# Optimization experiments

Hardware: AMD Instinct MI355X
Metric: run time of the kernel (lower is better)

## Reference

```python
import jax, jax.numpy as jnp
import numpy as np

N_HEAD = 50000
N_TAIL = 50000
E = 1600000
IN_F = 256
OUT_F = 32
NHEAD = 4
EDGE_F = 64
N_ETYPES = 5
NEG_SLOPE = 0.2


def setup_inputs() -> dict:
    key = jax.random.key(0)
    ks = jax.random.split(key, 10)
    return {
        "head_feature": jax.random.normal(ks[0], (N_HEAD, IN_F), jnp.float32),
        "tail_feature": jax.random.normal(ks[1], (N_TAIL, IN_F), jnp.float32),
        "W": jax.random.normal(ks[2], (IN_F, OUT_F * NHEAD), jnp.float32) * 0.05,
        "W_e": jax.random.normal(ks[3], (EDGE_F, EDGE_F * NHEAD), jnp.float32) * 0.05,
        "edge_emb": jax.random.normal(ks[4], (N_ETYPES, EDGE_F), jnp.float32) * 0.1,
        "a_l": jax.random.normal(ks[5], (1, NHEAD, OUT_F), jnp.float32) * 0.1,
        "a_r": jax.random.normal(ks[6], (1, NHEAD, OUT_F), jnp.float32) * 0.1,
        "a_e": jax.random.normal(ks[7], (1, NHEAD, EDGE_F), jnp.float32) * 0.1,
        "edge_list": jax.random.randint(ks[8], (2, E), 0, N_HEAD, jnp.int64),
        "tmp_edge": jax.random.randint(ks[9], (E,), 0, N_ETYPES, jnp.int64),
    }


def reference(head_feature, tail_feature, W, W_e, edge_emb, a_l, a_r, a_e, edge_list, tmp_edge):
    n_head_nodes = head_feature.shape[0]
    nhead, out_dim = a_l.shape[1], a_l.shape[2]
    edge_feats = a_e.shape[2]

    # dense projections (dropout in eval mode = identity)
    h_head = (head_feature @ W).reshape(-1, nhead, out_dim)   # [Nh, H, D]
    h_tail = (tail_feature @ W).reshape(-1, nhead, out_dim)   # [Nt, H, D]
    e = (edge_emb @ W_e).reshape(-1, nhead, edge_feats)       # [T,  H, De]

    head_ind = edge_list[0]
    tail_ind = edge_list[1]

    # per-edge attention logits [E, H]
    h_e = (a_e * e).sum(-1)[tmp_edge]
    h_l = (a_l * h_head).sum(-1)[head_ind]
    h_r = (a_r * h_tail).sum(-1)[tail_ind]
    att = jax.nn.leaky_relu(h_l + h_r + h_e, negative_slope=NEG_SLOPE)

    # sparse softmax over dim=1 (per head-node row), per head
    m = jax.ops.segment_max(att, head_ind, num_segments=n_head_nodes)
    m = jnp.where(jnp.isfinite(m), m, jnp.zeros_like(m))  # empty rows
    ex = jnp.exp(att - m[head_ind])
    denom = jax.ops.segment_sum(ex, head_ind, num_segments=n_head_nodes)
    alpha = ex / denom[head_ind]                              # [E, H]

    # sparse-mm aggregation: out[i] = sum_e alpha_e * h_tail[tail_e]
    msg = alpha[..., None] * h_tail[tail_ind]                 # [E, H, D]
    out = jax.ops.segment_sum(msg, head_ind, num_segments=n_head_nodes)
    out = out.reshape(n_head_nodes, nhead * out_dim)
    out = jax.nn.elu(out)
    return out, alpha
```

## Files before the change

### kernel.cpp

```cpp
#include <hip/hip_runtime.h>
#include <hip/hip_bf16.h>
#include <string.h>

#define NNODE 50000
#define NEDGE 1600000
#define INF   256
#define NH    4
#define EF    64
#define NET   5

#define NBUCK 782
#define BCAP  2560
#define EPB   2048
#define PBLK  782
#define BKS   784
#define RDB   1563

typedef unsigned short u16t;
typedef __attribute__((ext_vector_type(8))) short short8;
typedef __attribute__((ext_vector_type(4))) float f32x4;

__device__ __forceinline__ float b2f(u16t u) {
    union { unsigned int i; float f; } v; v.i = ((unsigned int)u) << 16; return v.f;
}
__device__ __forceinline__ u16t f2b(float f) {
    __hip_bfloat16 h = __float2bfloat16(f);
    u16t u; memcpy(&u, &h, 2); return u;
}

__global__ void k_detect(const int* __restrict__ el, const int* __restrict__ ety,
                         int* __restrict__ flag) {
    int tid = threadIdx.x;
    int w = tid >> 6, lane = tid & 63;
    const int* p = (w == 0) ? el : ety;
    int x = p[2 * lane + 1];
    unsigned long long b = __ballot(x != 0);
    if (lane == 0) flag[w] = (b == 0ULL) ? 1 : 0;
}

__global__ void k_prep(const float* __restrict__ W, const float* __restrict__ We,
                       const float* __restrict__ emb, const float* __restrict__ al,
                       const float* __restrict__ ar, const float* __restrict__ ae,
                       float* __restrict__ wl, float* __restrict__ wr,
                       float* __restrict__ he) {
    __shared__ float wes[EF * NH];
    int tid = threadIdx.x;
    {
        int k = tid;
        for (int h = 0; h < NH; h++) {
            float accl = 0.f, accr = 0.f;
            for (int d = 0; d < 32; d++) {
                float w = W[k * 128 + h * 32 + d];
                accl += w * al[h * 32 + d];
                accr += w * ar[h * 32 + d];
            }
            wl[k * NH + h] = accl;
            wr[k * NH + h] = accr;
        }
    }
    if (tid < EF) {
        int k = tid;
        for (int h = 0; h < NH; h++) {
            float s = 0.f;
            for (int d = 0; d < EF; d++)
                s += We[k * (NH * EF) + h * EF + d] * ae[h * EF + d];
            wes[k * NH + h] = s;
        }
    }
    __syncthreads();
    if (tid < NET * NH) {
        int t = tid / NH, h = tid % NH;
        float s = 0.f;
        for (int k = 0; k < EF; k++)
            s += emb[t * EF + k] * wes[k * NH + h];
        he[tid] = s;
    }
}

__global__ void k_prepw(const float* __restrict__ W, u16t* __restrict__ Wfrag) {
    int idx = blockIdx.x * 256 + threadIdx.x;
    int j    = idx & 7;
    int lane = (idx >> 3) & 63;
    int ks   = (idx >> 9) & 7;
    int tile = idx >> 12;
    int n = tile * 16 + (lane & 15);
    int k = ks * 32 + (lane >> 4) * 8 + j;
    Wfrag[idx] = f2b(W[k * 128 + n]);
}

__global__ void k_fuseA(const float* __restrict__ head, const float* __restrict__ tail,
                        const float* __restrict__ wl, const float* __restrict__ wr,
                        const int* __restrict__ el, const int* __restrict__ ety,
                        const int* __restrict__ flag,
                        int* __restrict__ hist2d, int* __restrict__ loff2d,
                        unsigned int* __restrict__ bucketbuf,
                        float* __restrict__ hl, float* __restrict__ hr) {
    __shared__ unsigned int srec[EPB];
    __shared__ int hist[BKS];
    __shared__ int loff[BKS];
    __shared__ int psum[256];
    int b = blockIdx.x;
    int tid = threadIdx.x;
    if (b < PBLK) {
        int base = b * EPB;
        int wf = flag[0], wt = flag[1];
        for (int i = tid; i < BKS; i += 256) hist[i] = 0;
        __syncthreads();
        unsigned int rec[8];
        unsigned int br[8];
#pragma unroll
        for (int i = 0; i < 8; i++) {
            int e = base + i * 256 + tid;
            br[i] = 0xffffffffu;
            rec[i] = 0;
            if (e < NEDGE) {
                int hi = wf ? el[2 * (long long)e]           : el[e];
                int ti = wf ? el[2 * ((long long)NEDGE + e)] : el[NEDGE + e];
                int ty = wt ? ety[2 * (long long)e]          : ety[e];
                int bk = hi >> 6;
                int r = atomicAdd(&hist[bk], 1);
                rec[i] = (unsigned)ti | ((unsigned)(hi & 63) << 16) | ((unsigned)ty << 22);
                br[i]  = (unsigned)bk | ((unsigned)r << 16);
            }
        }
        __syncthreads();
        int s4[4]; int tsum = 0;
        if (tid < 196) {
#pragma unroll
            for (int j = 0; j < 4; j++) { s4[j] = hist[4 * tid + j]; tsum += s4[j]; }
        }
        psum[tid] = (tid < 196) ? tsum : 0;
        __syncthreads();
        for (int off = 1; off < 256; off <<= 1) {
            int v = (tid >= off) ? psum[tid - off] : 0;
            __syncthreads();
            psum[tid] += v;
            __syncthreads();
        }
        if (tid < 196) {
            int run = tid ? psum[tid - 1] : 0;
#pragma unroll
            for (int j = 0; j < 4; j++) {
                int bk = 4 * tid + j;
                loff[bk] = run;
                hist2d[b * BKS + bk] = s4[j];
                loff2d[b * BKS + bk] = run;
                run += s4[j];
            }
        }
        __syncthreads();
#pragma unroll
        for (int i = 0; i < 8; i++) {
            if (br[i] != 0xffffffffu) {
                int bk = br[i] & 0xffff;
                int r  = br[i] >> 16;
                srec[loff[bk] + r] = rec[i];
            }
        }
        __syncthreads();
        int tot = psum[255];
        for (int i = tid; i < tot; i += 256)
            bucketbuf[(size_t)b * EPB + i] = srec[i];
    } else {
        int bb = b - PBLK;
        int ishead = (bb < RDB);
        const float* X  = ishead ? head : tail;
        const float* wv = ishead ? wl : wr;
        float* o        = ishead ? hl : hr;
        int rowbase = (ishead ? bb : bb - RDB) * 32;
        int wave = tid >> 6;
        int g = (tid >> 4) & 3;
        int l = tid & 15;
        const float4* wv4 = (const float4*)wv;
        float4 acc[2];
#pragma unroll
        for (int rr = 0; rr < 2; rr++) {
            acc[rr].x = 0.f; acc[rr].y = 0.f; acc[rr].z = 0.f; acc[rr].w = 0.f;
            int row = rowbase + rr * 16 + wave * 4 + g;
            if (row < NNODE) {
                const float* xp = X + (size_t)row * INF + l * 4;
#pragma unroll
                for (int c = 0; c < 4; c++) {
                    float4 xv = *(const float4*)(xp + c * 64);
                    float xs[4] = {xv.x, xv.y, xv.z, xv.w};
#pragma unroll
                    for (int j = 0; j < 4; j++) {
                        float4 wvv = wv4[c * 64 + l * 4 + j];
                        acc[rr].x += xs[j] * wvv.x;
                        acc[rr].y += xs[j] * wvv.y;
                        acc[rr].z += xs[j] * wvv.z;
                        acc[rr].w += xs[j] * wvv.w;
                    }
                }
            }
        }
#pragma unroll
        for (int rr = 0; rr < 2; rr++) {
#pragma unroll
            for (int off = 8; off > 0; off >>= 1) {
                acc[rr].x += __shfl_xor(acc[rr].x, off);
                acc[rr].y += __shfl_xor(acc[rr].y, off);
                acc[rr].z += __shfl_xor(acc[rr].z, off);
                acc[rr].w += __shfl_xor(acc[rr].w, off);
            }
            int row = rowbase + rr * 16 + wave * 4 + g;
            if (l == 0 && row < NNODE) ((float4*)o)[row] = acc[rr];
        }
    }
}

__global__ void k_bsum(const int* __restrict__ hist2d, int* __restrict__ cursor) {
    __shared__ int red[256];
    int bk = blockIdx.x;
    int tid = threadIdx.x;
    int s = 0;
    for (int sb = tid; sb < PBLK; sb += 256) s += hist2d[sb * BKS + bk];
    red[tid] = s;
    __syncthreads();
    for (int off = 128; off > 0; off >>= 1) {
        if (tid < off) red[tid] += red[tid + off];
        __syncthreads();
    }
    if (tid == 0) cursor[bk] = red[0];
}

__global__ void k_bscan(const int* __restrict__ cursor, int* __restrict__ bstart,
                        int* __restrict__ row_start) {
    __shared__ int psum[256];
    int tid = threadIdx.x;
    int s4[4]; int tsum = 0;
    if (tid < 196) {
#pragma unroll
        for (int j = 0; j < 4; j++) {
            int bk = 4 * tid + j;
            s4[j] = (bk < NBUCK) ? cursor[bk] : 0;
            tsum += s4[j];
        }
    }
    psum[tid] = (tid < 196) ? tsum : 0;
    __syncthreads();
    for (int off = 1; off < 256; off <<= 1) {
        int v = (tid >= off) ? psum[tid - off] : 0;
        __syncthreads();
        psum[tid] += v;
        __syncthreads();
    }
    if (tid < 196) {
        int run = tid ? psum[tid - 1] : 0;
#pragma unroll
        for (int j = 0; j < 4; j++) {
            int bk = 4 * tid + j;
            if (bk < NBUCK) bstart[bk] = run;
            run += s4[j];
        }
    }
    if (tid == 255) {
        bstart[NBUCK] = psum[255];
        row_start[NNODE] = psum[255];
    }
}

__global__ void k_fuseB(const float* __restrict__ X, const u16t* __restrict__ Wfrag,
                        u16t* __restrict__ H, const unsigned int* __restrict__ bucketbuf,
                        const int* __restrict__ hist2d, const int* __restrict__ loff2d,
                        const int* __restrict__ bstart,
                        unsigned int* __restrict__ cpack, int* __restrict__ row_start) {
    __shared__ __attribute__((aligned(16))) u16t alds[16 * 264];
    __shared__ unsigned int lrec[BCAP];
    __shared__ unsigned int lord[BCAP];
    __shared__ int psum[256];
    __shared__ int cnt[64];
    __shared__ int sc[64];
    int b = blockIdx.x;
    int tid = threadIdx.x;
    if (b < 3125) {
        int rowbase = b * 16;
        for (int i = tid; i < 1024; i += 256) {
            int row = i >> 6;
            int kc = (i & 63) * 4;
            float4 v = *(const float4*)(X + (size_t)(rowbase + row) * INF + kc);
            u16t* d = alds + row * 264 + kc;
            d[0] = f2b(v.x); d[1] = f2b(v.y); d[2] = f2b(v.z); d[3] = f2b(v.w);
        }
        __syncthreads();
        int wave = tid >> 6, lane = tid & 63;
        int m = lane & 15, quad = lane >> 4;
        int t0 = wave * 2, t1 = t0 + 1;
        f32x4 acc0 = {0.f, 0.f, 0.f, 0.f};
        f32x4 acc1 = {0.f, 0.f, 0.f, 0.f};
#pragma unroll
        for (int ks = 0; ks < 8; ks++) {
            short8 a  = *(const short8*)(alds + m * 264 + ks * 32 + quad * 8);
            short8 b0 = *(const short8*)(Wfrag + (((t0 * 8 + ks) * 64 + lane) << 3));
            short8 b1 = *(const short8*)(Wfrag + (((t1 * 8 + ks) * 64 + lane) << 3));
            acc0 = __builtin_amdgcn_mfma_f32_16x16x32_bf16(a, b0, acc0, 0, 0, 0);
            acc1 = __builtin_amdgcn_mfma_f32_16x16x32_bf16(a, b1, acc1, 0, 0, 0);
        }
        u16t* Hp = H + (size_t)rowbase * 128;
#pragma unroll
        for (int r = 0; r < 4; r++) {
            int row = quad * 4 + r;
            Hp[(size_t)row * 128 + t0 * 16 + m] = f2b(acc0[r]);
            Hp[(size_t)row * 128 + t1 * 16 + m] = f2b(acc1[r]);
        }
    } else {
        int q = b - 3125;
        int bs = bstart[q];
        int c4[4], o4[4]; int tsum = 0;
        if (tid < 196) {
#pragma unroll
            for (int j = 0; j < 4; j++) {
                int sb = 4 * tid + j;
                c4[j] = 0; o4[j] = 0;
                if (sb < PBLK) {
                    c4[j] = hist2d[sb * BKS + q];
                    o4[j] = loff2d[sb * BKS + q];
                }
                tsum += c4[j];
            }
        }
        psum[tid] = (tid < 196) ? tsum : 0;
        __syncthreads();
        for (int off = 1; off < 256; off <<= 1) {
            int v = (tid >= off) ? psum[tid - off] : 0;
            __syncthreads();
            psum[tid] += v;
            __syncthreads();
        }
        if (tid < 196) {
            int run = tid ? psum[tid - 1] : 0;
#pragma unroll
            for (int j = 0; j < 4; j++) {
                int sb = 4 * tid + j;
                for (int k = 0; k < c4[j]; k++) {
                    int d = run + k;
                    if (d < BCAP)
                        lrec[d] = bucketbuf[(size_t)sb * EPB + o4[j] + k];
                }
                run += c4[j];
            }
        }
        if (tid < 64) cnt[tid] = 0;
        __syncthreads();
        int nrec = psum[255];
        if (nrec > BCAP) nrec = BCAP;
        unsigned int myr[10];
        int k2 = 0;
        for (int i = tid; i < nrec; i += 256) {
            int n = (lrec[i] >> 16) & 63;
            myr[k2++] = atomicAdd(&cnt[n], 1);
        }
        __syncthreads();
        if (tid < 64) sc[tid] = cnt[tid];
        __syncthreads();
        for (int off = 1; off < 64; off <<= 1) {
            int v = (tid >= off && tid < 64) ? sc[tid - off] : 0;
            __syncthreads();
            if (tid < 64) sc[tid] += v;
            __syncthreads();
        }
        k2 = 0;
        for (int i = tid; i < nrec; i += 256) {
            unsigned int rc = lrec[i];
            int n  = (rc >> 16) & 63;
            int ti = rc & 0xffff;
            int ty = rc >> 22;
            int pos = (sc[n] - cnt[n]) + (int)myr[k2++];
            lord[pos] = ((unsigned)ty << 18) | (unsigned)ti;
        }
        __syncthreads();
        for (int i = tid; i < nrec; i += 256)
            cpack[bs + i] = lord[i];
        if (tid < 64) {
            int node = q * 64 + tid;
            if (node < NNODE) row_start[node] = bs + (sc[tid] - cnt[tid]);
        }
    }
}

__global__ void k_agg(const int* __restrict__ rs, const unsigned int* __restrict__ cpack,
                      const float* __restrict__ hl, const float* __restrict__ hr,
                      const float* __restrict__ heg, const u16t* __restrict__ ht,
                      float* __restrict__ den, float2* __restrict__ out) {
    __shared__ float hes[NET * NH];
    int tid = threadIdx.x;
    if (tid < NET * NH) hes[tid] = heg[tid];
    __syncthreads();
    int wave = tid >> 6, lane = tid & 63;
    int node = blockIdx.x * 4 + wave;
    int start = rs[node], end = rs[node + 1];
    unsigned h = (unsigned)(lane >> 4);
    unsigned lane2 = (unsigned)(lane << 1);
    float hlv = hl[(unsigned)node * 4u + h];
    const float* hesh = hes + h;
    float a0 = 0.f, a1 = 0.f, s = 0.f;
    int j = start;
    for (; j + 4 <= end; j += 4) {
        unsigned c0 = cpack[j], c1 = cpack[j + 1], c2 = cpack[j + 2], c3 = cpack[j + 3];
        unsigned t0 = c0 & 0xffffu, t1 = c1 & 0xffffu;
        unsigned t2 = c2 & 0xffffu, t3 = c3 & 0xffffu;
        float r0 = hr[(t0 << 2) + h], r1 = hr[(t1 << 2) + h];
        float r2 = hr[(t2 << 2) + h], r3 = hr[(t3 << 2) + h];
        unsigned v0 = *(const unsigned*)(ht + ((t0 << 7) + lane2));
        unsigned v1 = *(const unsigned*)(ht + ((t1 << 7) + lane2));
        unsigned v2 = *(const unsigned*)(ht + ((t2 << 7) + lane2));
        unsigned v3 = *(const unsigned*)(ht + ((t3 << 7) + lane2));
        float x0 = hlv + r0 + hesh[c0 >> 16];
        float x1 = hlv + r1 + hesh[c1 >> 16];
        float x2 = hlv + r2 + hesh[c2 >> 16];
        float x3 = hlv + r3 + hesh[c3 >> 16];
        x0 = fmaxf(x0, 0.2f * x0);
        x1 = fmaxf(x1, 0.2f * x1);
        x2 = fmaxf(x2, 0.2f * x2);
        x3 = fmaxf(x3, 0.2f * x3);
        float e0 = __expf(x0), e1 = __expf(x1), e2 = __expf(x2), e3 = __expf(x3);
        union { unsigned u; float f; } w0, w1;
        w0.u = v0 << 16;          w1.u = v0 & 0xffff0000u;
        a0 += e0 * w0.f;          a1 += e0 * w1.f;
        w0.u = v1 << 16;          w1.u = v1 & 0xffff0000u;
        a0 += e1 * w0.f;          a1 += e1 * w1.f;
        w0.u = v2 << 16;          w1.u = v2 & 0xffff0000u;
        a0 += e2 * w0.f;          a1 += e2 * w1.f;
        w0.u = v3 << 16;          w1.u = v3 & 0xffff0000u;
        a0 += e3 * w0.f;          a1 += e3 * w1.f;
        s  += e0 + e1 + e2 + e3;
    }
    for (; j < end; j++) {
        unsigned c = cpack[j];
        unsigned ti = c & 0xffffu;
        float att = hlv + hr[(ti << 2) + h] + hesh[c >> 16];
        att = fmaxf(att, 0.2f * att);
        float exv = __expf(att);
        unsigned hv = *(const unsigned*)(ht + ((ti << 7) + lane2));
        union { unsigned u; float f; } w0, w1;
        w0.u = hv << 16;  w1.u = hv & 0xffff0000u;
        a0 += exv * w0.f;
        a1 += exv * w1.f;
        s  += exv;
    }
    if ((lane & 15) == 0) den[(unsigned)node * 4u + h] = s;
    float o0 = 0.f, o1 = 0.f;
    if (s > 0.f) { o0 = a0 / s; o1 = a1 / s; }
    o0 = o0 > 0.f ? o0 : expm1f(o0);
    o1 = o1 > 0.f ? o1 : expm1f(o1);
    float2 ov = {o0, o1};
    out[(size_t)node * 64 + lane] = ov;
}

__global__ void k_alpha(const int* __restrict__ el, const int* __restrict__ ety,
                        const int* __restrict__ flag,
                        const float* __restrict__ hl, const float* __restrict__ hr,
                        const float* __restrict__ heg, const float* __restrict__ den,
                        float* __restrict__ alpha) {
    __shared__ float hes[NET * NH];
    int tid = threadIdx.x;
    if (tid < NET * NH) hes[tid] = heg[tid];
    __syncthreads();
    int wf = flag[0], wt = flag[1];
    int e = blockIdx.x * 256 + tid;
    int hi = wf ? el[2 * (long long)e]           : el[e];
    int ti = wf ? el[2 * ((long long)NEDGE + e)] : el[NEDGE + e];
    int ty = wt ? ety[2 * (long long)e]          : ety[e];
    float4 l = ((const float4*)hl)[hi];
    float4 r = ((const float4*)hr)[ti];
    float4 d = ((const float4*)den)[hi];
    float v0 = l.x + r.x + hes[ty * 4 + 0];
    float v1 = l.y + r.y + hes[ty * 4 + 1];
    float v2 = l.z + r.z + hes[ty * 4 + 2];
    float v3 = l.w + r.w + hes[ty * 4 + 3];
    v0 = v0 > 0.f ? v0 : 0.2f * v0;
    v1 = v1 > 0.f ? v1 : 0.2f * v1;
    v2 = v2 > 0.f ? v2 : 0.2f * v2;
    v3 = v3 > 0.f ? v3 : 0.2f * v3;
    float4 o;
    o.x = d.x > 0.f ? __expf(v0) / d.x : 0.f;
    o.y = d.y > 0.f ? __expf(v1) / d.y : 0.f;
    o.z = d.z > 0.f ? __expf(v2) / d.z : 0.f;
    o.w = d.w > 0.f ? __expf(v3) / d.w : 0.f;
    ((float4*)alpha)[e] = o;
}

extern "C" void kernel_launch(void* const* d_in, const int* in_sizes, int n_in,
                              void* d_out, int out_size, void* d_ws, size_t ws_size,
                              hipStream_t stream) {
    const float* head = (const float*)d_in[0];
    const float* tail = (const float*)d_in[1];
    const float* W    = (const float*)d_in[2];
    const float* We   = (const float*)d_in[3];
    const float* emb  = (const float*)d_in[4];
    const float* al   = (const float*)d_in[5];
    const float* ar   = (const float*)d_in[6];
    const float* ae   = (const float*)d_in[7];
    const int*   el   = (const int*)d_in[8];
    const int*   ety  = (const int*)d_in[9];

    float* ws = (float*)d_ws;
    float* hl       = ws;
    float* hr       = ws + 200000;
    float* wl       = ws + 400000;
    float* wr       = ws + 401024;
    float* heg      = ws + 402048;
    int*   flag     = (int*)(ws + 402080);
    int*   bstart   = (int*)(ws + 402096);
    int*   cursor   = (int*)(ws + 402880);
    float* den      = ws + 403664;
    int*   row_start= (int*)(ws + 603664);
    u16t*  Wfrag    = (u16t*)(ws + 653668);

    float* outp   = (float*)d_out;
    float* alphap = (float*)d_out + 6400000;
    u16t*         htail = (u16t*)alphap;
    unsigned int* cpack = (unsigned int*)(alphap + 3200000);
    unsigned int* bucketbuf = (unsigned int*)outp;
    int* hist2d = (int*)outp + 1601536;
    int* loff2d = hist2d + 613088;

    k_detect<<<1, 128, 0, stream>>>(el, ety, flag);
    k_prep<<<1, 256, 0, stream>>>(W, We, emb, al, ar, ae, wl, wr, heg);
    k_prepw<<<128, 256, 0, stream>>>(W, Wfrag);
    k_fuseA<<<PBLK + 2 * RDB, 256, 0, stream>>>(head, tail, wl, wr, el, ety, flag,
                                                hist2d, loff2d, bucketbuf, hl, hr);
    k_bsum<<<NBUCK, 256, 0, stream>>>(hist2d, cursor);
    k_bscan<<<1, 256, 0, stream>>>(cursor, bstart, row_start);
    k_fuseB<<<3125 + NBUCK, 256, 0, stream>>>(tail, Wfrag, htail, bucketbuf,
                                              hist2d, loff2d, bstart, cpack, row_start);
    k_agg<<<NNODE / 4, 256, 0, stream>>>(row_start, cpack, hl, hr, heg, htail,
                                         den, (float2*)outp);
    k_alpha<<<NEDGE / 256, 256, 0, stream>>>(el, ety, flag, hl, hr, heg, den, alphap);
}
```

Before: 338.4 us.

## Merge prep kernels and compute tail logits from the MFMA projection output

The three small setup kernels (flag detection, logit-weight prep, W fragment packing) are merged into one launch with block-specialised roles. The tail-node attention term hr is no longer computed by a separate pass over tail_feature in k_fuseA. Instead k_fuseB takes the dot product of a_r with the MFMA accumulators it already holds, cutting one full read of tail features and two launches. The catch is that hr is now derived from a bf16-input projection rather than fp32, which slightly changes numerics.

```diff
diff --git a/kernel.cpp b/kernel.cpp
--- a/kernel.cpp
+++ b/kernel.cpp
@@ -28,73 +28,74 @@
     u16t u; memcpy(&u, &h, 2); return u;
 }
 
-__global__ void k_detect(const int* __restrict__ el, const int* __restrict__ ety,
-                         int* __restrict__ flag) {
-    int tid = threadIdx.x;
-    int w = tid >> 6, lane = tid & 63;
-    const int* p = (w == 0) ? el : ety;
-    int x = p[2 * lane + 1];
-    unsigned long long b = __ballot(x != 0);
-    if (lane == 0) flag[w] = (b == 0ULL) ? 1 : 0;
-}
-
-__global__ void k_prep(const float* __restrict__ W, const float* __restrict__ We,
-                       const float* __restrict__ emb, const float* __restrict__ al,
-                       const float* __restrict__ ar, const float* __restrict__ ae,
-                       float* __restrict__ wl, float* __restrict__ wr,
-                       float* __restrict__ he) {
-    __shared__ float wes[EF * NH];
-    int tid = threadIdx.x;
-    {
-        int k = tid;
-        for (int h = 0; h < NH; h++) {
-            float accl = 0.f, accr = 0.f;
-            for (int d = 0; d < 32; d++) {
-                float w = W[k * 128 + h * 32 + d];
-                accl += w * al[h * 32 + d];
-                accr += w * ar[h * 32 + d];
-            }
-            wl[k * NH + h] = accl;
-            wr[k * NH + h] = accr;
-        }
-    }
-    if (tid < EF) {
-        int k = tid;
-        for (int h = 0; h < NH; h++) {
+__global__ void k_pre(const float* __restrict__ W, const float* __restrict__ We,
+                      const float* __restrict__ emb, const float* __restrict__ al,
+                      const float* __restrict__ ar, const float* __restrict__ ae,
+                      const int* __restrict__ el, const int* __restrict__ ety,
+                      float* __restrict__ wl, float* __restrict__ wr,
+                      float* __restrict__ he, int* __restrict__ flag,
+                      u16t* __restrict__ Wfrag) {
+    int b = blockIdx.x;
+    int tid = threadIdx.x;
+    if (b == 0) {
+        if (tid < 128) {
+            int w = tid >> 6, lane = tid & 63;
+            const int* p = (w == 0) ? el : ety;
+            int x = p[2 * lane + 1];
+            unsigned long long bal = __ballot(x != 0);
+            if (lane == 0) flag[w] = (bal == 0ULL) ? 1 : 0;
+        }
+    } else if (b == 1) {
+        __shared__ float wes[EF * NH];
+        {
+            int k = tid;
+            for (int h = 0; h < NH; h++) {
+                float accl = 0.f, accr = 0.f;
+                for (int d = 0; d < 32; d++) {
+                    float w = W[k * 128 + h * 32 + d];
+                    accl += w * al[h * 32 + d];
+                    accr += w * ar[h * 32 + d];
+                }
+                wl[k * NH + h] = accl;
+                wr[k * NH + h] = accr;
+            }
+        }
+        if (tid < EF) {
+            int k = tid;
+            for (int h = 0; h < NH; h++) {
+                float s = 0.f;
+                for (int d = 0; d < EF; d++)
+                    s += We[k * (NH * EF) + h * EF + d] * ae[h * EF + d];
+                wes[k * NH + h] = s;
+            }
+        }
+        __syncthreads();
+        if (tid < NET * NH) {
+            int t = tid / NH, h = tid % NH;
             float s = 0.f;
-            for (int d = 0; d < EF; d++)
-                s += We[k * (NH * EF) + h * EF + d] * ae[h * EF + d];
-            wes[k * NH + h] = s;
-        }
-    }
-    __syncthreads();
-    if (tid < NET * NH) {
-        int t = tid / NH, h = tid % NH;
-        float s = 0.f;
-        for (int k = 0; k < EF; k++)
-            s += emb[t * EF + k] * wes[k * NH + h];
-        he[tid] = s;
-    }
-}
-
-__global__ void k_prepw(const float* __restrict__ W, u16t* __restrict__ Wfrag) {
-    int idx = blockIdx.x * 256 + threadIdx.x;
-    int j    = idx & 7;
-    int lane = (idx >> 3) & 63;
-    int ks   = (idx >> 9) & 7;
-    int tile = idx >> 12;
-    int n = tile * 16 + (lane & 15);
-    int k = ks * 32 + (lane >> 4) * 8 + j;
-    Wfrag[idx] = f2b(W[k * 128 + n]);
-}
-
-__global__ void k_fuseA(const float* __restrict__ head, const float* __restrict__ tail,
-                        const float* __restrict__ wl, const float* __restrict__ wr,
+            for (int k = 0; k < EF; k++)
+                s += emb[t * EF + k] * wes[k * NH + h];
+            he[tid] = s;
+        }
+    } else {
+        int idx = (b - 2) * 256 + tid;
+        int j    = idx & 7;
+        int lane = (idx >> 3) & 63;
+        int ks   = (idx >> 9) & 7;
+        int tile = idx >> 12;
+        int n = tile * 16 + (lane & 15);
+        int k = ks * 32 + (lane >> 4) * 8 + j;
+        Wfrag[idx] = f2b(W[k * 128 + n]);
+    }
+}
+
+__global__ void k_fuseA(const float* __restrict__ head,
+                        const float* __restrict__ wl,
                         const int* __restrict__ el, const int* __restrict__ ety,
                         const int* __restrict__ flag,
                         int* __restrict__ hist2d, int* __restrict__ loff2d,
                         unsigned int* __restrict__ bucketbuf,
-                        float* __restrict__ hl, float* __restrict__ hr) {
+                        float* __restrict__ hl) {
     __shared__ unsigned int srec[EPB];
     __shared__ int hist[BKS];
     __shared__ int loff[BKS];
@@ -163,22 +164,18 @@
             bucketbuf[(size_t)b * EPB + i] = srec[i];
     } else {
         int bb = b - PBLK;
-        int ishead = (bb < RDB);
-        const float* X  = ishead ? head : tail;
-        const float* wv = ishead ? wl : wr;
-        float* o        = ishead ? hl : hr;
-        int rowbase = (ishead ? bb : bb - RDB) * 32;
+        int rowbase = bb * 32;
         int wave = tid >> 6;
         int g = (tid >> 4) & 3;
         int l = tid & 15;
-        const float4* wv4 = (const float4*)wv;
+        const float4* wv4 = (const float4*)wl;
         float4 acc[2];
 #pragma unroll
         for (int rr = 0; rr < 2; rr++) {
             acc[rr].x = 0.f; acc[rr].y = 0.f; acc[rr].z = 0.f; acc[rr].w = 0.f;
             int row = rowbase + rr * 16 + wave * 4 + g;
             if (row < NNODE) {
-                const float* xp = X + (size_t)row * INF + l * 4;
+                const float* xp = head + (size_t)row * INF + l * 4;
 #pragma unroll
                 for (int c = 0; c < 4; c++) {
                     float4 xv = *(const float4*)(xp + c * 64);
@@ -204,7 +201,7 @@
                 acc[rr].w += __shfl_xor(acc[rr].w, off);
             }
             int row = rowbase + rr * 16 + wave * 4 + g;
-            if (l == 0 && row < NNODE) ((float4*)o)[row] = acc[rr];
+            if (l == 0 && row < NNODE) ((float4*)hl)[row] = acc[rr];
         }
     }
 }
@@ -261,7 +258,9 @@
 }
 
 __global__ void k_fuseB(const float* __restrict__ X, const u16t* __restrict__ Wfrag,
-                        u16t* __restrict__ H, const unsigned int* __restrict__ bucketbuf,
+                        const float* __restrict__ ar,
+                        u16t* __restrict__ H, float* __restrict__ hr,
+                        const unsigned int* __restrict__ bucketbuf,
                         const int* __restrict__ hist2d, const int* __restrict__ loff2d,
                         const int* __restrict__ bstart,
                         unsigned int* __restrict__ cpack, int* __restrict__ row_start) {
@@ -302,6 +301,15 @@
             int row = quad * 4 + r;
             Hp[(size_t)row * 128 + t0 * 16 + m] = f2b(acc0[r]);
             Hp[(size_t)row * 128 + t1 * 16 + m] = f2b(acc1[r]);
+        }
+        float arm0 = ar[wave * 32 + m];
+        float arm1 = ar[wave * 32 + 16 + m];
+#pragma unroll
+        for (int r = 0; r < 4; r++) {
+            float p = arm0 * acc0[r] + arm1 * acc1[r];
+#pragma unroll
+            for (int off = 8; off > 0; off >>= 1) p += __shfl_xor(p, off);
+            if (m == 0) hr[(rowbase + quad * 4 + r) * 4 + wave] = p;
         }
     } else {
         int q = b - 3125;
@@ -515,14 +523,13 @@
     int* hist2d = (int*)outp + 1601536;
     int* loff2d = hist2d + 613088;
 
-    k_detect<<<1, 128, 0, stream>>>(el, ety, flag);
-    k_prep<<<1, 256, 0, stream>>>(W, We, emb, al, ar, ae, wl, wr, heg);
-    k_prepw<<<128, 256, 0, stream>>>(W, Wfrag);
-    k_fuseA<<<PBLK + 2 * RDB, 256, 0, stream>>>(head, tail, wl, wr, el, ety, flag,
-                                                hist2d, loff2d, bucketbuf, hl, hr);
+    k_pre<<<130, 256, 0, stream>>>(W, We, emb, al, ar, ae, el, ety,
+                                   wl, wr, heg, flag, Wfrag);
+    k_fuseA<<<PBLK + RDB, 256, 0, stream>>>(head, wl, el, ety, flag,
+                                            hist2d, loff2d, bucketbuf, hl);
     k_bsum<<<NBUCK, 256, 0, stream>>>(hist2d, cursor);
     k_bscan<<<1, 256, 0, stream>>>(cursor, bstart, row_start);
-    k_fuseB<<<3125 + NBUCK, 256, 0, stream>>>(tail, Wfrag, htail, bucketbuf,
+    k_fuseB<<<3125 + NBUCK, 256, 0, stream>>>(tail, Wfrag, ar, htail, hr, bucketbuf,
                                               hist2d, loff2d, bstart, cpack, row_start);
     k_agg<<<NNODE / 4, 256, 0, stream>>>(row_start, cpack, hl, hr, heg, htail,
                                          den, (float2*)outp);
```

New measurement: 326.0 us. -3.7%, faster.
